# Performance work log

Measured on AMD Instinct MI355X. Metric: run time of the kernel, lower is better.

## Reference

```python
import jax, jax.numpy as jnp
import numpy as np

B, NCLS, P, C, D, H, DIMG = 256, 1000, 5, 72, 512, 8, 768
T = P + C  # 77 = CLIP context length
DH = D // H


def _ln(x, g, b):
    m = jnp.mean(x, axis=-1, keepdims=True)
    v = jnp.var(x, axis=-1, keepdims=True)
    return (x - m) * jax.lax.rsqrt(v + 1e-5) * g + b


def _transformer(x, ln_g, ln_b, Wq, Wk, Wv, Wo):
    # Stand-in for clip.model.transformer: pre-LN self-attention block that
    # also exposes its (head-averaged) attention map, as used by
    # clip.get_attention_map(). x: [N, T, D]
    N, Tx, _ = x.shape
    h = _ln(x, ln_g, ln_b)
    q = (h @ Wq).reshape(N, Tx, H, DH)
    k = (h @ Wk).reshape(N, Tx, H, DH)
    v = (h @ Wv).reshape(N, Tx, H, DH)
    scores = jnp.einsum('nqhd,nkhd->nhqk', q, k) / jnp.sqrt(jnp.float32(DH))
    A = jax.nn.softmax(scores, axis=-1)          # [N, H, T, T]
    attn_map = A.mean(axis=1)                    # [N, T, T]
    o = jnp.einsum('nhqk,nkhd->nqhd', A, v).reshape(N, Tx, D) @ Wo
    return x + o, attn_map


def setup_inputs() -> dict:
    key = jax.random.key(0)
    ks = jax.random.split(key, 10)
    s = 0.02
    return {
        'images': jax.random.normal(ks[0], (B, DIMG), jnp.float32),
        'W_img': jax.random.normal(ks[1], (DIMG, D), jnp.float32) * s,
        'ctx': jax.random.normal(ks[2], (NCLS, P, D), jnp.float32) * s,
        'cls_tok': jax.random.normal(ks[3], (NCLS, C, D), jnp.float32) * s,
        'ln_g': jnp.ones((D,), jnp.float32),
        'ln_b': jnp.zeros((D,), jnp.float32),
        'Wq': jax.random.normal(ks[4], (D, D), jnp.float32) * s,
        'Wk': jax.random.normal(ks[5], (D, D), jnp.float32) * s,
        'Wv': jax.random.normal(ks[6], (D, D), jnp.float32) * s,
        'Wo': jax.random.normal(ks[7], (D, D), jnp.float32) * s,
        'text_proj': jax.random.normal(ks[8], (D, D), jnp.float32) * s,
        'logit_scale': jnp.full((1,), np.log(1.0 / 0.07), jnp.float32),
    }


def reference(images, W_img, ctx, cls_tok, ln_g, ln_b, Wq, Wk, Wv, Wo,
              text_proj, logit_scale):
    # Image branch: encode + L2 normalize
    img = images @ W_img
    img = img / jnp.linalg.norm(img, axis=-1, keepdims=True)  # [B, D]

    # Prompts are identical across the batch in the original (ctx.expand),
    # so the per-sample inner loop collapses to one pass per class.
    prompt = jnp.concatenate([ctx, cls_tok], axis=1)          # [NCLS, T, D]
    _, attn = _transformer(prompt, ln_g, ln_b, Wq, Wk, Wv, Wo)

    # AttributionMonitor: attention from the last (EOT) token onto the
    # prompt_len learned context tokens, normalized.
    attr = jax.nn.softmax(attn[:, -1, :P], axis=-1)           # [NCLS, P]

    # PromptAdjustor(method='scale'): scale context tokens by attribution.
    adj_ctx = ctx * attr[..., None]
    adj_prompt = jnp.concatenate([adj_ctx, cls_tok], axis=1)  # [NCLS, T, D]

    h, _ = _transformer(adj_prompt, ln_g, ln_b, Wq, Wk, Wv, Wo)
    txt = h[:, -1, :] @ text_proj                             # [NCLS, D]
    txt = txt / jnp.linalg.norm(txt, axis=-1, keepdims=True)

    logits = jnp.exp(logit_scale[0]) * (img @ txt.T)          # [B, NCLS]
    return logits
```

## Files before the change

### kernel.cpp

```cpp
#include <hip/hip_runtime.h>
#include <hip/hip_bf16.h>

#define DEV static __device__ __forceinline__

typedef __attribute__((ext_vector_type(8))) short bf16x8;
typedef __attribute__((ext_vector_type(4))) short s16x4;
typedef __attribute__((ext_vector_type(4))) float f32x4;

DEV float wsum(float v) {
  v += __shfl_xor(v, 1);  v += __shfl_xor(v, 2);  v += __shfl_xor(v, 4);
  v += __shfl_xor(v, 8);  v += __shfl_xor(v, 16); v += __shfl_xor(v, 32);
  return v;
}
DEV float wmaxr(float v) {
  v = fmaxf(v, __shfl_xor(v, 1));  v = fmaxf(v, __shfl_xor(v, 2));
  v = fmaxf(v, __shfl_xor(v, 4));  v = fmaxf(v, __shfl_xor(v, 8));
  v = fmaxf(v, __shfl_xor(v, 16)); v = fmaxf(v, __shfl_xor(v, 32));
  return v;
}
DEV short f2bf(float x) {
  __hip_bfloat16 h = __float2bfloat16(x);
  return *reinterpret_cast<short*>(&h);
}
DEV float bf2f(unsigned int u) {
  const unsigned int x = u << 16;
  return __uint_as_float(x);
}
DEV float bfs2f(short s) {
  const unsigned int x = ((unsigned int)(unsigned short)s) << 16;
  return __uint_as_float(x);
}

DEV float fold8(const float v[8], int lane) {
  float w4[4];
#pragma unroll
  for (int j = 0; j < 4; ++j) {
    const float mine  = (lane & 1) ? v[2 * j + 1] : v[2 * j];
    const float other = (lane & 1) ? v[2 * j]     : v[2 * j + 1];
    w4[j] = mine + __shfl_xor(other, 1);
  }
  float u2[2];
#pragma unroll
  for (int j = 0; j < 2; ++j) {
    const float mine  = (lane & 2) ? w4[2 * j + 1] : w4[2 * j];
    const float other = (lane & 2) ? w4[2 * j]     : w4[2 * j + 1];
    u2[j] = mine + __shfl_xor(other, 2);
  }
  const float mine  = (lane & 4) ? u2[1] : u2[0];
  const float other = (lane & 4) ? u2[0] : u2[1];
  float z = mine + __shfl_xor(other, 4);
  z += __shfl_xor(z, 8); z += __shfl_xor(z, 16); z += __shfl_xor(z, 32);
  return z;
}

template <int TRANSB, int ADDD, int ABF16, int OUTBF16>
__global__ __launch_bounds__(256) void gemm_mfma_k(
    const void* __restrict__ Av, int lda, long long bsA,
    const float* __restrict__ B, int ldb, long long bsB,
    void* __restrict__ Cv, int ldc, long long bsC,
    const float* __restrict__ D, long long ldd,
    int M, int N, int K)
{
  const float* Af = (const float*)Av + (ABF16 ? 0 : (size_t)blockIdx.z * bsA);
  const short* Ah = (const short*)Av + (ABF16 ? (size_t)blockIdx.z * bsA : 0);
  B += (size_t)blockIdx.z * bsB;
  const int m0 = blockIdx.y * 64, n0 = blockIdx.x * 64;
  const int tid = threadIdx.x;
  const int w = tid >> 6, lane = tid & 63;
  const int wr = w >> 1, wc = w & 1;
  __shared__ __attribute__((aligned(16))) short As[2][64][40];
  __shared__ __attribute__((aligned(16))) short Bs[2][64][40];
  f32x4 acc[2][2] = {};

  const int ar = tid >> 2, akc = (tid & 3) * 8;
  const int br = tid >> 3, bnc = (tid & 7) * 8;
  const bool arv = (m0 + ar < M);
  const int rbase = wr * 32 + (lane & 15);
  const int cbase = wc * 32 + (lane & 15);
  const int kb = (lane >> 4) * 8;

  auto gload = [&](int k0, float4& a0, float4& a1, bf16x8& ah,
                   float4& b0, float4& b1) {
    if (ABF16) {
      ah = bf16x8{};
      if (arv) ah = *(const bf16x8*)(Ah + (size_t)(m0 + ar) * lda + k0 + akc);
    } else {
      a0 = make_float4(0.f, 0.f, 0.f, 0.f); a1 = a0;
      if (arv) {
        a0 = *(const float4*)(Af + (size_t)(m0 + ar) * lda + k0 + akc);
        a1 = *(const float4*)(Af + (size_t)(m0 + ar) * lda + k0 + akc + 4);
      }
    }
    if (TRANSB) {
      b0 = *(const float4*)(B + (size_t)(n0 + ar) * ldb + k0 + akc);
      b1 = *(const float4*)(B + (size_t)(n0 + ar) * ldb + k0 + akc + 4);
    } else {
      b0 = *(const float4*)(B + (size_t)(k0 + br) * ldb + n0 + bnc);
      b1 = *(const float4*)(B + (size_t)(k0 + br) * ldb + n0 + bnc + 4);
    }
  };
  auto stage = [&](int buf, const float4& a0, const float4& a1, const bf16x8& ah,
                   const float4& b0, const float4& b1) {
    if (ABF16) {
      *(bf16x8*)&As[buf][ar][akc] = ah;
    } else {
      bf16x8 av;
      av[0] = f2bf(a0.x); av[1] = f2bf(a0.y); av[2] = f2bf(a0.z); av[3] = f2bf(a0.w);
      av[4] = f2bf(a1.x); av[5] = f2bf(a1.y); av[6] = f2bf(a1.z); av[7] = f2bf(a1.w);
      *(bf16x8*)&As[buf][ar][akc] = av;
    }
    if (TRANSB) {
      bf16x8 bv;
      bv[0] = f2bf(b0.x); bv[1] = f2bf(b0.y); bv[2] = f2bf(b0.z); bv[3] = f2bf(b0.w);
      bv[4] = f2bf(b1.x); bv[5] = f2bf(b1.y); bv[6] = f2bf(b1.z); bv[7] = f2bf(b1.w);
      *(bf16x8*)&Bs[buf][ar][akc] = bv;
    } else {
      Bs[buf][bnc + 0][br] = f2bf(b0.x); Bs[buf][bnc + 1][br] = f2bf(b0.y);
      Bs[buf][bnc + 2][br] = f2bf(b0.z); Bs[buf][bnc + 3][br] = f2bf(b0.w);
      Bs[buf][bnc + 4][br] = f2bf(b1.x); Bs[buf][bnc + 5][br] = f2bf(b1.y);
      Bs[buf][bnc + 6][br] = f2bf(b1.z); Bs[buf][bnc + 7][br] = f2bf(b1.w);
    }
  };
  auto compute = [&](int buf) {
    bf16x8 af0 = *(const bf16x8*)&As[buf][rbase][kb];
    bf16x8 af1 = *(const bf16x8*)&As[buf][rbase + 16][kb];
    bf16x8 bf0 = *(const bf16x8*)&Bs[buf][cbase][kb];
    bf16x8 bf1 = *(const bf16x8*)&Bs[buf][cbase + 16][kb];
    acc[0][0] = __builtin_amdgcn_mfma_f32_16x16x32_bf16(af0, bf0, acc[0][0], 0, 0, 0);
    acc[0][1] = __builtin_amdgcn_mfma_f32_16x16x32_bf16(af0, bf1, acc[0][1], 0, 0, 0);
    acc[1][0] = __builtin_amdgcn_mfma_f32_16x16x32_bf16(af1, bf0, acc[1][0], 0, 0, 0);
    acc[1][1] = __builtin_amdgcn_mfma_f32_16x16x32_bf16(af1, bf1, acc[1][1], 0, 0, 0);
  };

  float4 a0A, a1A, b0A, b1A, a0B, a1B, b0B, b1B;
  bf16x8 ahA = {}, ahB = {};
  gload(0, a0A, a1A, ahA, b0A, b1A);
  gload(32, a0B, a1B, ahB, b0B, b1B);
  for (int k0 = 0; k0 < K; k0 += 64) {
    stage(0, a0A, a1A, ahA, b0A, b1A);
    if (k0 + 64 < K) gload(k0 + 64, a0A, a1A, ahA, b0A, b1A);
    __syncthreads();
    compute(0);
    stage(1, a0B, a1B, ahB, b0B, b1B);
    if (k0 + 96 < K) gload(k0 + 96, a0B, a1B, ahB, b0B, b1B);
    __syncthreads();
    compute(1);
  }

  const size_t cb = (size_t)blockIdx.z * (size_t)bsC;
#pragma unroll
  for (int mi = 0; mi < 2; ++mi)
#pragma unroll
    for (int ni = 0; ni < 2; ++ni)
#pragma unroll
      for (int r = 0; r < 4; ++r) {
        const int row = m0 + wr * 32 + mi * 16 + (lane >> 4) * 4 + r;
        const int col = n0 + wc * 32 + ni * 16 + (lane & 15);
        if (row < M) {
          float v = acc[mi][ni][r];
          if (ADDD) v += D[(size_t)row * ldd + col];
          if (OUTBF16)
            ((__hip_bfloat16*)Cv)[cb + (size_t)row * ldc + col] = __float2bfloat16(v);
          else
            ((float*)Cv)[cb + (size_t)row * ldc + col] = v;
        }
      }
}

__global__ __launch_bounds__(256) void gemm_mfma_lnA_k(
    const float* __restrict__ A, long long lda,
    const float* __restrict__ g, const float* __restrict__ b,
    const float* __restrict__ B, int ldb,
    float* __restrict__ C, int ldc,
    int M, int N, int K)
{
  const int m0 = blockIdx.y * 64, n0 = blockIdx.x * 64;
  const int tid = threadIdx.x;
  const int w = tid >> 6, lane = tid & 63;
  const int wr = w >> 1, wc = w & 1;
  __shared__ __attribute__((aligned(16))) short As[2][64][40];
  __shared__ __attribute__((aligned(16))) short Bs[2][64][40];
  __shared__ __attribute__((aligned(16))) float g_s[512], b_s[512];
  __shared__ float mean_s[64], rstd_s[64];
  f32x4 acc[2][2] = {};

  if (tid < 128) ((float4*)g_s)[tid] = ((const float4*)g)[tid];
  else ((float4*)b_s)[tid - 128] = ((const float4*)b)[tid - 128];

  {
    const int r = tid >> 2, p = tid & 3;
    float s = 0.f, ss = 0.f;
    if (m0 + r < M) {
      const float4* src = (const float4*)(A + (size_t)(m0 + r) * lda + p * 128);
#pragma unroll 8
      for (int i = 0; i < 32; ++i) {
        const float4 v = src[i];
        s += v.x + v.y + v.z + v.w;
        ss += v.x * v.x + v.y * v.y + v.z * v.z + v.w * v.w;
      }
    }
    s += __shfl_xor(s, 1);  s += __shfl_xor(s, 2);
    ss += __shfl_xor(ss, 1); ss += __shfl_xor(ss, 2);
    if (p == 0) {
      const float mean = s * (1.f / 512.f);
      mean_s[r] = mean;
      rstd_s[r] = rsqrtf(ss * (1.f / 512.f) - mean * mean + 1e-5f);
    }
  }
  __syncthreads();

  const int ar = tid >> 2, akc = (tid & 3) * 8;
  const int br = tid >> 3, bnc = (tid & 7) * 8;
  const bool arv = (m0 + ar < M);
  const int rbase = wr * 32 + (lane & 15);
  const int cbase = wc * 32 + (lane & 15);
  const int kb = (lane >> 4) * 8;

  auto gload = [&](int k0, float4& a0, float4& a1, float4& b0, float4& b1) {
    a0 = make_float4(0.f, 0.f, 0.f, 0.f); a1 = a0;
    if (arv) {
      a0 = *(const float4*)(A + (size_t)(m0 + ar) * lda + k0 + akc);
      a1 = *(const float4*)(A + (size_t)(m0 + ar) * lda + k0 + akc + 4);
    }
    b0 = *(const float4*)(B + (size_t)(k0 + br) * ldb + n0 + bnc);
    b1 = *(const float4*)(B + (size_t)(k0 + br) * ldb + n0 + bnc + 4);
  };
  auto stage = [&](int buf, int k0, const float4& a0, const float4& a1,
                   const float4& b0, const float4& b1) {
    const float mn = mean_s[ar], rs = rstd_s[ar];
    const int kc = k0 + akc;
    bf16x8 av;
    av[0] = f2bf((a0.x - mn) * rs * g_s[kc + 0] + b_s[kc + 0]);
    av[1] = f2bf((a0.y - mn) * rs * g_s[kc + 1] + b_s[kc + 1]);
    av[2] = f2bf((a0.z - mn) * rs * g_s[kc + 2] + b_s[kc + 2]);
    av[3] = f2bf((a0.w - mn) * rs * g_s[kc + 3] + b_s[kc + 3]);
    av[4] = f2bf((a1.x - mn) * rs * g_s[kc + 4] + b_s[kc + 4]);
    av[5] = f2bf((a1.y - mn) * rs * g_s[kc + 5] + b_s[kc + 5]);
    av[6] = f2bf((a1.z - mn) * rs * g_s[kc + 6] + b_s[kc + 6]);
    av[7] = f2bf((a1.w - mn) * rs * g_s[kc + 7] + b_s[kc + 7]);
    *(bf16x8*)&As[buf][ar][akc] = av;
    Bs[buf][bnc + 0][br] = f2bf(b0.x); Bs[buf][bnc + 1][br] = f2bf(b0.y);
    Bs[buf][bnc + 2][br] = f2bf(b0.z); Bs[buf][bnc + 3][br] = f2bf(b0.w);
    Bs[buf][bnc + 4][br] = f2bf(b1.x); Bs[buf][bnc + 5][br] = f2bf(b1.y);
    Bs[buf][bnc + 6][br] = f2bf(b1.z); Bs[buf][bnc + 7][br] = f2bf(b1.w);
  };
  auto compute = [&](int buf) {
    bf16x8 af0 = *(const bf16x8*)&As[buf][rbase][kb];
    bf16x8 af1 = *(const bf16x8*)&As[buf][rbase + 16][kb];
    bf16x8 bf0 = *(const bf16x8*)&Bs[buf][cbase][kb];
    bf16x8 bf1 = *(const bf16x8*)&Bs[buf][cbase + 16][kb];
    acc[0][0] = __builtin_amdgcn_mfma_f32_16x16x32_bf16(af0, bf0, acc[0][0], 0, 0, 0);
    acc[0][1] = __builtin_amdgcn_mfma_f32_16x16x32_bf16(af0, bf1, acc[0][1], 0, 0, 0);
    acc[1][0] = __builtin_amdgcn_mfma_f32_16x16x32_bf16(af1, bf0, acc[1][0], 0, 0, 0);
    acc[1][1] = __builtin_amdgcn_mfma_f32_16x16x32_bf16(af1, bf1, acc[1][1], 0, 0, 0);
  };

  float4 a0A, a1A, b0A, b1A, a0B, a1B, b0B, b1B;
  gload(0, a0A, a1A, b0A, b1A);
  gload(32, a0B, a1B, b0B, b1B);
  for (int k0 = 0; k0 < K; k0 += 64) {
    stage(0, k0, a0A, a1A, b0A, b1A);
    if (k0 + 64 < K) gload(k0 + 64, a0A, a1A, b0A, b1A);
    __syncthreads();
    compute(0);
    stage(1, k0 + 32, a0B, a1B, b0B, b1B);
    if (k0 + 96 < K) gload(k0 + 96, a0B, a1B, b0B, b1B);
    __syncthreads();
    compute(1);
  }

#pragma unroll
  for (int mi = 0; mi < 2; ++mi)
#pragma unroll
    for (int ni = 0; ni < 2; ++ni)
#pragma unroll
      for (int r = 0; r < 4; ++r) {
        const int row = m0 + wr * 32 + mi * 16 + (lane >> 4) * 4 + r;
        const int col = n0 + wc * 32 + ni * 16 + (lane & 15);
        if (row < M) C[(size_t)row * ldc + col] = acc[mi][ni][r];
      }
}

__global__ __launch_bounds__(256) void logits_k(
    const float* __restrict__ A, int lda,
    const float* __restrict__ B, int ldb,
    float* __restrict__ C, int ldc,
    const float* __restrict__ alpha_ptr,
    int M, int N, int K)
{
  const int m0 = blockIdx.y * 32, n0 = blockIdx.x * 64;
  const int tid = threadIdx.x;
  __shared__ __attribute__((aligned(16))) float As[2][16][36];
  __shared__ __attribute__((aligned(16))) float Bs[2][16][68];
  __shared__ float nA[32], nB[64];
  float acc[2][4] = {};
  float ssA = 0.f, ssB = 0.f;
  const int ty = tid >> 4, tx = tid & 15;
  const int am = tid >> 3, ak = (tid & 7) * 2;
  const int bm = tid >> 2, bt = (tid & 3) * 4;
  const bool aval = (m0 + am < M);
  const bool bval = (n0 + bm < N);

  float2 av; float4 bv;
  auto gload = [&](int k0) {
    av = make_float2(0.f, 0.f);
    bv = make_float4(0.f, 0.f, 0.f, 0.f);
    if (aval) av = *(const float2*)(A + (size_t)(m0 + am) * lda + (k0 + ak));
    if (bval) bv = *(const float4*)(B + (size_t)(n0 + bm) * ldb + (k0 + bt));
    ssA += av.x * av.x + av.y * av.y;
    ssB += bv.x * bv.x + bv.y * bv.y + bv.z * bv.z + bv.w * bv.w;
  };
  auto sstore = [&](int buf) {
    As[buf][ak][am] = av.x; As[buf][ak + 1][am] = av.y;
    Bs[buf][bt + 0][bm] = bv.x; Bs[buf][bt + 1][bm] = bv.y;
    Bs[buf][bt + 2][bm] = bv.z; Bs[buf][bt + 3][bm] = bv.w;
  };

  const int nIt = K >> 4;
  gload(0); sstore(0);
  for (int it = 0; it < nIt; ++it) {
    __syncthreads();
    if (it + 1 < nIt) gload((it + 1) << 4);
    const int buf = it & 1;
#pragma unroll
    for (int kk = 0; kk < 16; ++kk) {
      const float2 a  = *(const float2*)&As[buf][kk][ty * 2];
      const float4 bq = *(const float4*)&Bs[buf][kk][tx * 4];
      acc[0][0] += a.x * bq.x; acc[0][1] += a.x * bq.y; acc[0][2] += a.x * bq.z; acc[0][3] += a.x * bq.w;
      acc[1][0] += a.y * bq.x; acc[1][1] += a.y * bq.y; acc[1][2] += a.y * bq.z; acc[1][3] += a.y * bq.w;
    }
    if (it + 1 < nIt) sstore((it + 1) & 1);
  }

  ssA += __shfl_xor(ssA, 1); ssA += __shfl_xor(ssA, 2); ssA += __shfl_xor(ssA, 4);
  if ((tid & 7) == 0) nA[am] = rsqrtf(ssA);
  ssB += __shfl_xor(ssB, 1); ssB += __shfl_xor(ssB, 2);
  if ((tid & 3) == 0) nB[bm] = rsqrtf(ssB);
  __syncthreads();

  const float alpha = __expf(alpha_ptr[0]);
#pragma unroll
  for (int i = 0; i < 2; ++i) {
    const int m = m0 + ty * 2 + i;
    if (m >= M) continue;
    const float fa = alpha * nA[ty * 2 + i];
#pragma unroll
    for (int j = 0; j < 4; ++j) {
      const int nn = n0 + tx * 4 + j;
      if (nn < N) C[(size_t)m * ldc + nn] = acc[i][j] * fa * nB[tx * 4 + j];
    }
  }
}

__global__ __launch_bounds__(256) void fused_sweep_kernel(
    const float* __restrict__ ctx, const float* __restrict__ cls,
    const float* __restrict__ g, const float* __restrict__ b,
    const __hip_bfloat16* __restrict__ wt, __hip_bfloat16* __restrict__ u_out)
{
  const int n = blockIdx.x, tid = threadIdx.x;
  const int w = tid >> 6, lane = tid & 63;
  __shared__ __attribute__((aligned(16))) float gw_s[8][512];
  __shared__ __attribute__((aligned(16))) float g_s[512], b_s[512];
  __shared__ __attribute__((aligned(16))) short h2_s[5][512];
  __shared__ float sc_s[8][80];
  __shared__ float sc2_s[8][5];
  __shared__ float ah_s[8][5];
  __shared__ float wstatB[4][8], wstatL[4][8];
  __shared__ float attr_s[5];
  __shared__ float Sgw_l[8], bw_l[8];
  __shared__ float Bt_s[8], Lt_s[8], inv_s[8];
  __shared__ float e2_s[8][5];
  __shared__ __attribute__((aligned(16))) float es_s[4][2][8];

  {
    const uint4* wsrc = (const uint4*)(wt + (size_t)n * 4096);
    float4* gwf = (float4*)&gw_s[0][0];
    for (int i = tid; i < 512; i += 256) {
      const uint4 v = wsrc[i];
      gwf[i * 2]     = make_float4(bf2f(v.x & 0xffffu), bf2f(v.x >> 16),
                                   bf2f(v.y & 0xffffu), bf2f(v.y >> 16));
      gwf[i * 2 + 1] = make_float4(bf2f(v.z & 0xffffu), bf2f(v.z >> 16),
                                   bf2f(v.w & 0xffffu), bf2f(v.w >> 16));
    }
    if (tid < 128) ((float4*)g_s)[tid] = ((const float4*)g)[tid];
    else ((float4*)b_s)[tid - 128] = ((const float4*)b)[tid - 128];
  }
  __syncthreads();

  for (int hh = w; hh < 8; hh += 4) {
    float s1 = 0.f, s2 = 0.f;
#pragma unroll
    for (int i = 0; i < 8; ++i) {
      const int j = lane + 64 * i;
      const float wv = gw_s[hh][j];
      const float gv = wv * g_s[j];
      s1 += gv; s2 += wv * b_s[j];
      gw_s[hh][j] = gv;
    }
    s1 = wsum(s1); s2 = wsum(s2);
    if (lane == 0) { Sgw_l[hh] = s1; bw_l[hh] = s2; }
  }
  __syncthreads();
  const float sg_r  = Sgw_l[lane & 7];
  const float bw8_r = bw_l[lane & 7] * 0.125f;
  const int j0 = lane * 4, j1 = lane * 4 + 256;

  for (int k = w; k < 5; k += 4) {
    const float* src = ctx + ((size_t)n * 5 + k) * 512;
    const float4 x0 = *(const float4*)(src + j0);
    const float4 x1 = *(const float4*)(src + j1);
    float s  = x0.x + x0.y + x0.z + x0.w + x1.x + x1.y + x1.z + x1.w;
    float ss = x0.x * x0.x + x0.y * x0.y + x0.z * x0.z + x0.w * x0.w
             + x1.x * x1.x + x1.y * x1.y + x1.z * x1.z + x1.w * x1.w;
    float v8[8] = {};
#pragma unroll
    for (int hh = 0; hh < 8; ++hh) {
      const float4 w0 = *(const float4*)&gw_s[hh][j0];
      const float4 w1 = *(const float4*)&gw_s[hh][j1];
      v8[hh] = x0.x * w0.x + x0.y * w0.y + x0.z * w0.z + x0.w * w0.w
             + x1.x * w1.x + x1.y * w1.y + x1.z * w1.z + x1.w * w1.w;
    }
    s = wsum(s); ss = wsum(ss);
    const float mean = s * (1.f / 512.f);
    const float rstd = rsqrtf(ss * (1.f / 512.f) - mean * mean + 1e-5f);
    const float z = fold8(v8, lane);
    const float zf = rstd * 0.125f * (z - mean * sg_r) + bw8_r;
    if (lane < 8) sc_s[lane][k] = zf;
  }

  float A[8][8];
#pragma unroll
  for (int hh = 0; hh < 8; ++hh)
#pragma unroll
    for (int i = 0; i < 8; ++i) A[hh][i] = 0.f;
  float B8[8] = {}, L8[8] = {};

  const float* base = cls + (size_t)n * 72 * 512;
  float4 xa0, xa1, xb0, xb1, ya0, ya1, yb0, yb1;
  {
    const float* sA = base + (size_t)w * 512;
    const float* sB = base + (size_t)(w + 4) * 512;
    xa0 = *(const float4*)(sA + j0); xa1 = *(const float4*)(sA + j1);
    xb0 = *(const float4*)(sB + j0); xb1 = *(const float4*)(sB + j1);
    const float* sA1 = base + (size_t)(w + 8) * 512;
    const float* sB1 = base + (size_t)(w + 12) * 512;
    ya0 = *(const float4*)(sA1 + j0); ya1 = *(const float4*)(sA1 + j1);
    yb0 = *(const float4*)(sB1 + j0); yb1 = *(const float4*)(sB1 + j1);
  }
  for (int p = 0; p < 9; ++p) {
    float4 za0, za1, zb0, zb1;
    const bool more2 = (p + 2 < 9);
    if (more2) {
      const float* sA = base + (size_t)(w + 8 * (p + 2)) * 512;
      const float* sB = base + (size_t)(w + 4 + 8 * (p + 2)) * 512;
      za0 = *(const float4*)(sA + j0); za1 = *(const float4*)(sA + j1);
      zb0 = *(const float4*)(sB + j0); zb1 = *(const float4*)(sB + j1);
    }
    float sa = xa0.x + xa0.y + xa0.z + xa0.w + xa1.x + xa1.y + xa1.z + xa1.w;
    float ssa = xa0.x * xa0.x + xa0.y * xa0.y + xa0.z * xa0.z + xa0.w * xa0.w
              + xa1.x * xa1.x + xa1.y * xa1.y + xa1.z * xa1.z + xa1.w * xa1.w;
    float sb = xb0.x + xb0.y + xb0.z + xb0.w + xb1.x + xb1.y + xb1.z + xb1.w;
    float ssb = xb0.x * xb0.x + xb0.y * xb0.y + xb0.z * xb0.z + xb0.w * xb0.w
              + xb1.x * xb1.x + xb1.y * xb1.y + xb1.z * xb1.z + xb1.w * xb1.w;
    float v8a[8], v8b[8];
#pragma unroll
    for (int hh = 0; hh < 8; ++hh) {
      const float4 w0 = *(const float4*)&gw_s[hh][j0];
      const float4 w1 = *(const float4*)&gw_s[hh][j1];
      v8a[hh] = xa0.x * w0.x + xa0.y * w0.y + xa0.z * w0.z + xa0.w * w0.w
              + xa1.x * w1.x + xa1.y * w1.y + xa1.z * w1.z + xa1.w * w1.w;
      v8b[hh] = xb0.x * w0.x + xb0.y * w0.y + xb0.z * w0.z + xb0.w * w0.w
              + xb1.x * w1.x + xb1.y * w1.y + xb1.z * w1.z + xb1.w * w1.w;
    }
    sa = wsum(sa); ssa = wsum(ssa); sb = wsum(sb); ssb = wsum(ssb);
    const float meanA = sa * (1.f / 512.f);
    const float rstdA = rsqrtf(ssa * (1.f / 512.f) - meanA * meanA + 1e-5f);
    const float meanB = sb * (1.f / 512.f);
    const float rstdB = rsqrtf(ssb * (1.f / 512.f) - meanB * meanB + 1e-5f);
    const float za = fold8(v8a, lane);
    const float zb = fold8(v8b, lane);
    const float zfa = rstdA * 0.125f * (za - meanA * sg_r) + bw8_r;
    const float zfb = rstdB * 0.125f * (zb - meanB * sg_r) + bw8_r;
    const int kA = 5 + w + 8 * p;
    if (lane < 8) {
      sc_s[lane][kA] = zfa; sc_s[lane][kA + 4] = zfb;
      es_s[w][0][lane] = __expf(zfa);
      es_s[w][1][lane] = __expf(zfb);
    }
    __builtin_amdgcn_wave_barrier();
    const float4 ea0 = *(const float4*)&es_s[w][0][0];
    const float4 ea1 = *(const float4*)&es_s[w][0][4];
    const float4 eb0 = *(const float4*)&es_s[w][1][0];
    const float4 eb1 = *(const float4*)&es_s[w][1][4];
    const float esa[8] = {ea0.x, ea0.y, ea0.z, ea0.w, ea1.x, ea1.y, ea1.z, ea1.w};
    const float esb[8] = {eb0.x, eb0.y, eb0.z, eb0.w, eb1.x, eb1.y, eb1.z, eb1.w};
#pragma unroll
    for (int hh = 0; hh < 8; ++hh) {
      const float erA = esa[hh] * rstdA;
      const float erB = esb[hh] * rstdB;
      A[hh][0] += erA * xa0.x; A[hh][1] += erA * xa0.y;
      A[hh][2] += erA * xa0.z; A[hh][3] += erA * xa0.w;
      A[hh][4] += erA * xa1.x; A[hh][5] += erA * xa1.y;
      A[hh][6] += erA * xa1.z; A[hh][7] += erA * xa1.w;
      B8[hh] += erA * meanA;
      L8[hh] += esa[hh];
      A[hh][0] += erB * xb0.x; A[hh][1] += erB * xb0.y;
      A[hh][2] += erB * xb0.z; A[hh][3] += erB * xb0.w;
      A[hh][4] += erB * xb1.x; A[hh][5] += erB * xb1.y;
      A[hh][6] += erB * xb1.z; A[hh][7] += erB * xb1.w;
      B8[hh] += erB * meanB;
      L8[hh] += esb[hh];
    }
    xa0 = ya0; xa1 = ya1; xb0 = yb0; xb1 = yb1;
    if (more2) { ya0 = za0; ya1 = za1; yb0 = zb0; yb1 = zb1; }
  }
  if (lane == 0)
#pragma unroll
    for (int hh = 0; hh < 8; ++hh) {
      wstatB[w][hh] = B8[hh]; wstatL[w][hh] = L8[hh];
    }
  __syncthreads();

  for (int hh = w; hh < 8; hh += 4) {
    const float v0 = sc_s[hh][lane];
    const float v1 = (lane + 64 < 77) ? sc_s[hh][lane + 64] : -1e30f;
    const float mx = wmaxr(fmaxf(v0, v1));
    const float e0 = __expf(v0 - mx);
    const float e1 = (lane + 64 < 77) ? __expf(v1 - mx) : 0.f;
    const float S = wsum(e0 + e1);
    if (lane < 5) ah_s[hh][lane] = e0 / S;
  }
  __syncthreads();
  if (tid == 0) {
    float m[5], mx = -1e30f;
#pragma unroll
    for (int p = 0; p < 5; ++p) {
      float acc = 0.f;
      for (int hh = 0; hh < 8; ++hh) acc += ah_s[hh][p];
      m[p] = acc * 0.125f;
      mx = fmaxf(mx, m[p]);
    }
    float e[5], S = 0.f;
#pragma unroll
    for (int p = 0; p < 5; ++p) { e[p] = __expf(m[p] - mx); S += e[p]; }
#pragma unroll
    for (int p = 0; p < 5; ++p) attr_s[p] = e[p] / S;
  }
  __syncthreads();

  for (int k = w; k < 5; k += 4) {
    const float c = attr_s[k];
    const float* src = ctx + ((size_t)n * 5 + k) * 512;
    float4 x0 = *(const float4*)(src + j0);
    float4 x1 = *(const float4*)(src + j1);
    x0.x *= c; x0.y *= c; x0.z *= c; x0.w *= c;
    x1.x *= c; x1.y *= c; x1.z *= c; x1.w *= c;
    float s  = x0.x + x0.y + x0.z + x0.w + x1.x + x1.y + x1.z + x1.w;
    float ss = x0.x * x0.x + x0.y * x0.y + x0.z * x0.z + x0.w * x0.w
             + x1.x * x1.x + x1.y * x1.y + x1.z * x1.z + x1.w * x1.w;
    float v8[8];
#pragma unroll
    for (int hh = 0; hh < 8; ++hh) {
      const float4 w0 = *(const float4*)&gw_s[hh][j0];
      const float4 w1 = *(const float4*)&gw_s[hh][j1];
      v8[hh] = x0.x * w0.x + x0.y * w0.y + x0.z * w0.z + x0.w * w0.w
             + x1.x * w1.x + x1.y * w1.y + x1.z * w1.z + x1.w * w1.w;
    }
    s = wsum(s); ss = wsum(ss);
    const float mean = s * (1.f / 512.f);
    const float rstd = rsqrtf(ss * (1.f / 512.f) - mean * mean + 1e-5f);
    {
      const float4 gg0 = *(const float4*)&g_s[j0];
      const float4 bb0 = *(const float4*)&b_s[j0];
      const float4 gg1 = *(const float4*)&g_s[j1];
      const float4 bb1 = *(const float4*)&b_s[j1];
      s16x4 o0, o1;
      o0[0] = f2bf((x0.x - mean) * rstd * gg0.x + bb0.x);
      o0[1] = f2bf((x0.y - mean) * rstd * gg0.y + bb0.y);
      o0[2] = f2bf((x0.z - mean) * rstd * gg0.z + bb0.z);
      o0[3] = f2bf((x0.w - mean) * rstd * gg0.w + bb0.w);
      o1[0] = f2bf((x1.x - mean) * rstd * gg1.x + bb1.x);
      o1[1] = f2bf((x1.y - mean) * rstd * gg1.y + bb1.y);
      o1[2] = f2bf((x1.z - mean) * rstd * gg1.z + bb1.z);
      o1[3] = f2bf((x1.w - mean) * rstd * gg1.w + bb1.w);
      *(s16x4*)&h2_s[k][j0] = o0;
      *(s16x4*)&h2_s[k][j1] = o1;
    }
    const float z = fold8(v8, lane);
    const float zf = rstd * 0.125f * (z - mean * sg_r) + bw8_r;
    if (lane < 8) sc2_s[lane][k] = zf;
  }
  __syncthreads();

  for (int wv = 0; wv < 4; ++wv) {
    if (w == wv) {
#pragma unroll
      for (int hh = 0; hh < 8; ++hh) {
        float4* p0 = (float4*)&gw_s[hh][j0];
        float4* p1 = (float4*)&gw_s[hh][j1];
        const float4 a0 = make_float4(A[hh][0], A[hh][1], A[hh][2], A[hh][3]);
        const float4 a1 = make_float4(A[hh][4], A[hh][5], A[hh][6], A[hh][7]);
        if (wv == 0) { *p0 = a0; *p1 = a1; }
        else {
          float4 v0 = *p0, v1 = *p1;
          v0.x += a0.x; v0.y += a0.y; v0.z += a0.z; v0.w += a0.w;
          v1.x += a1.x; v1.y += a1.y; v1.z += a1.z; v1.w += a1.w;
          *p0 = v0; *p1 = v1;
        }
      }
    }
    __syncthreads();
  }

  if (tid < 8) {
    float Bt = 0.f, Lt = 0.f;
    for (int wv = 0; wv < 4; ++wv) { Bt += wstatB[wv][tid]; Lt += wstatL[wv][tid]; }
    float den = Lt;
#pragma unroll
    for (int k = 0; k < 5; ++k) {
      const float e = __expf(sc2_s[tid][k]);
      e2_s[tid][k] = e; den += e;
    }
    Bt_s[tid] = Bt; Lt_s[tid] = Lt; inv_s[tid] = 1.f / den;
  }
  __syncthreads();

  __hip_bfloat16* dst = u_out + (size_t)n * 4096;
  for (int bidx = tid * 4; bidx < 4096; bidx += 1024) {
    const int hh = bidx >> 9, j = bidx & 511;
    const float4 a4 = *(const float4*)&gw_s[hh][j];
    const float4 g4 = *(const float4*)&g_s[j];
    const float4 b4 = *(const float4*)&b_s[j];
    const float Bt = Bt_s[hh], Lt = Lt_s[hh];
    float v0 = (a4.x - Bt) * g4.x + Lt * b4.x;
    float v1 = (a4.y - Bt) * g4.y + Lt * b4.y;
    float v2 = (a4.z - Bt) * g4.z + Lt * b4.z;
    float v3 = (a4.w - Bt) * g4.w + Lt * b4.w;
#pragma unroll
    for (int k = 0; k < 5; ++k) {
      const s16x4 hq = *(const s16x4*)&h2_s[k][j];
      const float e = e2_s[hh][k];
      v0 += e * bfs2f(hq[0]); v1 += e * bfs2f(hq[1]);
      v2 += e * bfs2f(hq[2]); v3 += e * bfs2f(hq[3]);
    }
    const float iv = inv_s[hh];
    s16x4 o;
    o[0] = f2bf(v0 * iv); o[1] = f2bf(v1 * iv);
    o[2] = f2bf(v2 * iv); o[3] = f2bf(v3 * iv);
    *(s16x4*)&dst[bidx] = o;
  }
}

extern "C" void kernel_launch(void* const* d_in, const int* in_sizes, int n_in,
                              void* d_out, int out_size, void* d_ws, size_t ws_size,
                              hipStream_t stream)
{
  const float* images = (const float*)d_in[0];
  const float* W_img  = (const float*)d_in[1];
  const float* ctx    = (const float*)d_in[2];
  const float* cls    = (const float*)d_in[3];
  const float* ln_g   = (const float*)d_in[4];
  const float* ln_b   = (const float*)d_in[5];
  const float* Wq     = (const float*)d_in[6];
  const float* Wk     = (const float*)d_in[7];
  const float* Wv     = (const float*)d_in[8];
  const float* Wo     = (const float*)d_in[9];
  const float* tproj  = (const float*)d_in[10];
  const float* lscale = (const float*)d_in[11];

  __hip_bfloat16* wtu = (__hip_bfloat16*)d_ws;
  float* fws  = (float*)d_ws;
  float* img  = fws + 2048000;
  float* hlO  = img + 131072;
  float* qo2  = hlO + 512000;
  float* txt  = fws;
  (void)in_sizes; (void)n_in; (void)out_size; (void)ws_size;

  gemm_mfma_k<0,0,0,0><<<dim3(8,4,1),256,0,stream>>>(images,768,0, W_img,512,0,
      img,512,0, nullptr,0, 256,512,768);

  gemm_mfma_lnA_k<<<dim3(8,16),256,0,stream>>>(cls + 71*512, 72*512,
      ln_g, ln_b, Wq,512, qo2,512, 1000,512,512);

  gemm_mfma_k<1,0,0,1><<<dim3(8,16,8),256,0,stream>>>(qo2,512,64, Wk,512,64,
      wtu,4096,512, nullptr,0, 1000,512,64);

  fused_sweep_kernel<<<1000,256,0,stream>>>(ctx, cls, ln_g, ln_b, wtu, wtu);

  gemm_mfma_k<0,0,1,0><<<dim3(1,16,8),256,0,stream>>>(wtu,4096,512, Wv,512,64,
      hlO,512,64, nullptr,0, 1000,64,512);

  gemm_mfma_k<0,1,0,0><<<dim3(8,16,1),256,0,stream>>>(hlO,512,0, Wo,512,0,
      qo2,512,0, cls + 71*512, 72*512, 1000,512,512);
  gemm_mfma_k<0,0,0,0><<<dim3(8,16,1),256,0,stream>>>(qo2,512,0, tproj,512,0,
      txt,512,0, nullptr,0, 1000,512,512);

  logits_k<<<dim3(16,8),256,0,stream>>>(img,512, txt,512,
      (float*)d_out,1000, lscale, 256,1000,512);
}
```

Before: 154.0 us.

## Stage gamma-scaled prompt rows in LDS and compute EOT scores with MFMA

The fused per-class sweep kernel now loads all 77 prompt rows once into shared memory as bf16, pre-multiplied by the LayerNorm gamma, and stores per-row mean and rstd. The EOT-query attention scores are then computed with 16x16x32 bf16 MFMA instructions instead of per-row wave reductions. The second pass reuses the cached rows rather than re-reading global memory, and derives the scaled-context LayerNorm statistics analytically from the first pass's values. The trade-off is a large LDS footprint (about 80x516 shorts), which may reduce occupancy, plus bf16 rounding of gamma*x that costs some accuracy.

```diff
diff --git a/kernel.cpp b/kernel.cpp
--- a/kernel.cpp
+++ b/kernel.cpp
@@ -6,6 +6,7 @@
 typedef __attribute__((ext_vector_type(8))) short bf16x8;
 typedef __attribute__((ext_vector_type(4))) short s16x4;
 typedef __attribute__((ext_vector_type(4))) float f32x4;
+typedef __attribute__((ext_vector_type(2))) float f32x2;
 
 DEV float wsum(float v) {
   v += __shfl_xor(v, 1);  v += __shfl_xor(v, 2);  v += __shfl_xor(v, 4);
@@ -29,28 +30,6 @@
 DEV float bfs2f(short s) {
   const unsigned int x = ((unsigned int)(unsigned short)s) << 16;
   return __uint_as_float(x);
-}
-
-DEV float fold8(const float v[8], int lane) {
-  float w4[4];
-#pragma unroll
-  for (int j = 0; j < 4; ++j) {
-    const float mine  = (lane & 1) ? v[2 * j + 1] : v[2 * j];
-    const float other = (lane & 1) ? v[2 * j]     : v[2 * j + 1];
-    w4[j] = mine + __shfl_xor(other, 1);
-  }
-  float u2[2];
-#pragma unroll
-  for (int j = 0; j < 2; ++j) {
-    const float mine  = (lane & 2) ? w4[2 * j + 1] : w4[2 * j];
-    const float other = (lane & 2) ? w4[2 * j]     : w4[2 * j + 1];
-    u2[j] = mine + __shfl_xor(other, 2);
-  }
-  const float mine  = (lane & 4) ? u2[1] : u2[0];
-  const float other = (lane & 4) ? u2[0] : u2[1];
-  float z = mine + __shfl_xor(other, 4);
-  z += __shfl_xor(z, 8); z += __shfl_xor(z, 16); z += __shfl_xor(z, 32);
-  return z;
 }
 
 template <int TRANSB, int ADDD, int ABF16, int OUTBF16>
@@ -359,10 +338,14 @@
 {
   const int n = blockIdx.x, tid = threadIdx.x;
   const int w = tid >> 6, lane = tid & 63;
-  __shared__ __attribute__((aligned(16))) float gw_s[8][512];
+  constexpr int XP = 516;
+  __shared__ __attribute__((aligned(16))) short Xs[80][XP];
   __shared__ __attribute__((aligned(16))) float g_s[512], b_s[512];
   __shared__ __attribute__((aligned(16))) short h2_s[5][512];
+  __shared__ float mean_s[80], rstd_s[80];
   __shared__ float sc_s[8][80];
+  __shared__ float es_s[8][72];
+  __shared__ float zraw_s[8][5];
   __shared__ float sc2_s[8][5];
   __shared__ float ah_s[8][5];
   __shared__ float wstatB[4][8], wstatL[4][8];
@@ -370,155 +353,81 @@
   __shared__ float Sgw_l[8], bw_l[8];
   __shared__ float Bt_s[8], Lt_s[8], inv_s[8];
   __shared__ float e2_s[8][5];
-  __shared__ __attribute__((aligned(16))) float es_s[4][2][8];
-
-  {
-    const uint4* wsrc = (const uint4*)(wt + (size_t)n * 4096);
-    float4* gwf = (float4*)&gw_s[0][0];
-    for (int i = tid; i < 512; i += 256) {
-      const uint4 v = wsrc[i];
-      gwf[i * 2]     = make_float4(bf2f(v.x & 0xffffu), bf2f(v.x >> 16),
-                                   bf2f(v.y & 0xffffu), bf2f(v.y >> 16));
-      gwf[i * 2 + 1] = make_float4(bf2f(v.z & 0xffffu), bf2f(v.z >> 16),
-                                   bf2f(v.w & 0xffffu), bf2f(v.w >> 16));
-    }
-    if (tid < 128) ((float4*)g_s)[tid] = ((const float4*)g)[tid];
-    else ((float4*)b_s)[tid - 128] = ((const float4*)b)[tid - 128];
-  }
-  __syncthreads();
-
-  for (int hh = w; hh < 8; hh += 4) {
-    float s1 = 0.f, s2 = 0.f;
-#pragma unroll
-    for (int i = 0; i < 8; ++i) {
-      const int j = lane + 64 * i;
-      const float wv = gw_s[hh][j];
-      const float gv = wv * g_s[j];
-      s1 += gv; s2 += wv * b_s[j];
-      gw_s[hh][j] = gv;
-    }
-    s1 = wsum(s1); s2 = wsum(s2);
-    if (lane == 0) { Sgw_l[hh] = s1; bw_l[hh] = s2; }
-  }
-  __syncthreads();
-  const float sg_r  = Sgw_l[lane & 7];
-  const float bw8_r = bw_l[lane & 7] * 0.125f;
-  const int j0 = lane * 4, j1 = lane * 4 + 256;
-
-  for (int k = w; k < 5; k += 4) {
-    const float* src = ctx + ((size_t)n * 5 + k) * 512;
-    const float4 x0 = *(const float4*)(src + j0);
-    const float4 x1 = *(const float4*)(src + j1);
-    float s  = x0.x + x0.y + x0.z + x0.w + x1.x + x1.y + x1.z + x1.w;
-    float ss = x0.x * x0.x + x0.y * x0.y + x0.z * x0.z + x0.w * x0.w
-             + x1.x * x1.x + x1.y * x1.y + x1.z * x1.z + x1.w * x1.w;
-    float v8[8] = {};
-#pragma unroll
-    for (int hh = 0; hh < 8; ++hh) {
-      const float4 w0 = *(const float4*)&gw_s[hh][j0];
-      const float4 w1 = *(const float4*)&gw_s[hh][j1];
-      v8[hh] = x0.x * w0.x + x0.y * w0.y + x0.z * w0.z + x0.w * w0.w
-             + x1.x * w1.x + x1.y * w1.y + x1.z * w1.z + x1.w * w1.w;
-    }
-    s = wsum(s); ss = wsum(ss);
-    const float mean = s * (1.f / 512.f);
-    const float rstd = rsqrtf(ss * (1.f / 512.f) - mean * mean + 1e-5f);
-    const float z = fold8(v8, lane);
-    const float zf = rstd * 0.125f * (z - mean * sg_r) + bw8_r;
-    if (lane < 8) sc_s[lane][k] = zf;
-  }
-
-  float A[8][8];
-#pragma unroll
-  for (int hh = 0; hh < 8; ++hh)
-#pragma unroll
-    for (int i = 0; i < 8; ++i) A[hh][i] = 0.f;
-  float B8[8] = {}, L8[8] = {};
-
-  const float* base = cls + (size_t)n * 72 * 512;
-  float4 xa0, xa1, xb0, xb1, ya0, ya1, yb0, yb1;
-  {
-    const float* sA = base + (size_t)w * 512;
-    const float* sB = base + (size_t)(w + 4) * 512;
-    xa0 = *(const float4*)(sA + j0); xa1 = *(const float4*)(sA + j1);
-    xb0 = *(const float4*)(sB + j0); xb1 = *(const float4*)(sB + j1);
-    const float* sA1 = base + (size_t)(w + 8) * 512;
-    const float* sB1 = base + (size_t)(w + 12) * 512;
-    ya0 = *(const float4*)(sA1 + j0); ya1 = *(const float4*)(sA1 + j1);
-    yb0 = *(const float4*)(sB1 + j0); yb1 = *(const float4*)(sB1 + j1);
-  }
-  for (int p = 0; p < 9; ++p) {
-    float4 za0, za1, zb0, zb1;
-    const bool more2 = (p + 2 < 9);
-    if (more2) {
-      const float* sA = base + (size_t)(w + 8 * (p + 2)) * 512;
-      const float* sB = base + (size_t)(w + 4 + 8 * (p + 2)) * 512;
-      za0 = *(const float4*)(sA + j0); za1 = *(const float4*)(sA + j1);
-      zb0 = *(const float4*)(sB + j0); zb1 = *(const float4*)(sB + j1);
-    }
-    float sa = xa0.x + xa0.y + xa0.z + xa0.w + xa1.x + xa1.y + xa1.z + xa1.w;
-    float ssa = xa0.x * xa0.x + xa0.y * xa0.y + xa0.z * xa0.z + xa0.w * xa0.w
-              + xa1.x * xa1.x + xa1.y * xa1.y + xa1.z * xa1.z + xa1.w * xa1.w;
-    float sb = xb0.x + xb0.y + xb0.z + xb0.w + xb1.x + xb1.y + xb1.z + xb1.w;
-    float ssb = xb0.x * xb0.x + xb0.y * xb0.y + xb0.z * xb0.z + xb0.w * xb0.w
-              + xb1.x * xb1.x + xb1.y * xb1.y + xb1.z * xb1.z + xb1.w * xb1.w;
-    float v8a[8], v8b[8];
-#pragma unroll
-    for (int hh = 0; hh < 8; ++hh) {
-      const float4 w0 = *(const float4*)&gw_s[hh][j0];
-      const float4 w1 = *(const float4*)&gw_s[hh][j1];
-      v8a[hh] = xa0.x * w0.x + xa0.y * w0.y + xa0.z * w0.z + xa0.w * w0.w
-              + xa1.x * w1.x + xa1.y * w1.y + xa1.z * w1.z + xa1.w * w1.w;
-      v8b[hh] = xb0.x * w0.x + xb0.y * w0.y + xb0.z * w0.z + xb0.w * w0.w
-              + xb1.x * w1.x + xb1.y * w1.y + xb1.z * w1.z + xb1.w * w1.w;
-    }
-    sa = wsum(sa); ssa = wsum(ssa); sb = wsum(sb); ssb = wsum(ssb);
-    const float meanA = sa * (1.f / 512.f);
-    const float rstdA = rsqrtf(ssa * (1.f / 512.f) - meanA * meanA + 1e-5f);
-    const float meanB = sb * (1.f / 512.f);
-    const float rstdB = rsqrtf(ssb * (1.f / 512.f) - meanB * meanB + 1e-5f);
-    const float za = fold8(v8a, lane);
-    const float zb = fold8(v8b, lane);
-    const float zfa = rstdA * 0.125f * (za - meanA * sg_r) + bw8_r;
-    const float zfb = rstdB * 0.125f * (zb - meanB * sg_r) + bw8_r;
-    const int kA = 5 + w + 8 * p;
-    if (lane < 8) {
-      sc_s[lane][kA] = zfa; sc_s[lane][kA + 4] = zfb;
-      es_s[w][0][lane] = __expf(zfa);
-      es_s[w][1][lane] = __expf(zfb);
-    }
-    __builtin_amdgcn_wave_barrier();
-    const float4 ea0 = *(const float4*)&es_s[w][0][0];
-    const float4 ea1 = *(const float4*)&es_s[w][0][4];
-    const float4 eb0 = *(const float4*)&es_s[w][1][0];
-    const float4 eb1 = *(const float4*)&es_s[w][1][4];
-    const float esa[8] = {ea0.x, ea0.y, ea0.z, ea0.w, ea1.x, ea1.y, ea1.z, ea1.w};
-    const float esb[8] = {eb0.x, eb0.y, eb0.z, eb0.w, eb1.x, eb1.y, eb1.z, eb1.w};
-#pragma unroll
-    for (int hh = 0; hh < 8; ++hh) {
-      const float erA = esa[hh] * rstdA;
-      const float erB = esb[hh] * rstdB;
-      A[hh][0] += erA * xa0.x; A[hh][1] += erA * xa0.y;
-      A[hh][2] += erA * xa0.z; A[hh][3] += erA * xa0.w;
-      A[hh][4] += erA * xa1.x; A[hh][5] += erA * xa1.y;
-      A[hh][6] += erA * xa1.z; A[hh][7] += erA * xa1.w;
-      B8[hh] += erA * meanA;
-      L8[hh] += esa[hh];
-      A[hh][0] += erB * xb0.x; A[hh][1] += erB * xb0.y;
-      A[hh][2] += erB * xb0.z; A[hh][3] += erB * xb0.w;
-      A[hh][4] += erB * xb1.x; A[hh][5] += erB * xb1.y;
-      A[hh][6] += erB * xb1.z; A[hh][7] += erB * xb1.w;
-      B8[hh] += erB * meanB;
-      L8[hh] += esb[hh];
-    }
-    xa0 = ya0; xa1 = ya1; xb0 = yb0; xb1 = yb1;
-    if (more2) { ya0 = za0; ya1 = za1; yb0 = zb0; yb1 = zb1; }
-  }
-  if (lane == 0)
-#pragma unroll
-    for (int hh = 0; hh < 8; ++hh) {
-      wstatB[w][hh] = B8[hh]; wstatL[w][hh] = L8[hh];
-    }
+
+  if (tid < 128) ((float4*)g_s)[tid] = ((const float4*)g)[tid];
+  else ((float4*)b_s)[tid - 128] = ((const float4*)b)[tid - 128];
+  __syncthreads();
+
+  const short* wtS = (const short*)wt + (size_t)n * 4096;
+
+  auto loadrow = [&](int row, int p) {
+    const float* src = (row < 5)
+        ? ctx + ((size_t)n * 5 + row) * 512 + p * 128
+        : cls + ((size_t)n * 72 + (row - 5)) * 512 + p * 128;
+    float s = 0.f, ss = 0.f;
+    for (int c2 = 0; c2 < 4; ++c2) {
+      float4 xv[8];
+#pragma unroll
+      for (int i = 0; i < 8; ++i) xv[i] = ((const float4*)src)[c2 * 8 + i];
+#pragma unroll
+      for (int i = 0; i < 8; ++i) {
+        s  += xv[i].x + xv[i].y + xv[i].z + xv[i].w;
+        ss += xv[i].x * xv[i].x + xv[i].y * xv[i].y
+            + xv[i].z * xv[i].z + xv[i].w * xv[i].w;
+        const int j = p * 128 + c2 * 32 + i * 4;
+        const float4 gg = *(const float4*)&g_s[j];
+        s16x4 o;
+        o[0] = f2bf(xv[i].x * gg.x); o[1] = f2bf(xv[i].y * gg.y);
+        o[2] = f2bf(xv[i].z * gg.z); o[3] = f2bf(xv[i].w * gg.w);
+        *(s16x4*)&Xs[row][j] = o;
+      }
+    }
+    s += __shfl_xor(s, 1);  s += __shfl_xor(s, 2);
+    ss += __shfl_xor(ss, 1); ss += __shfl_xor(ss, 2);
+    if (p == 0) {
+      const float mean = s * (1.f / 512.f);
+      mean_s[row] = mean;
+      rstd_s[row] = rsqrtf(ss * (1.f / 512.f) - mean * mean + 1e-5f);
+    }
+  };
+  loadrow(tid >> 2, tid & 3);
+  if (tid < 52) {
+    loadrow(64 + (tid >> 2), tid & 3);
+  } else if (w >= 1) {
+    for (int h = w - 1; h < 8; h += 3) {
+      const bf16x8 wv = *(const bf16x8*)(wtS + h * 512 + lane * 8);
+      float s1 = 0.f, s2 = 0.f;
+#pragma unroll
+      for (int i = 0; i < 8; ++i) {
+        const float wf = bfs2f(wv[i]);
+        s1 += wf * g_s[lane * 8 + i];
+        s2 += wf * b_s[lane * 8 + i];
+      }
+      s1 = wsum(s1); s2 = wsum(s2);
+      if (lane == 0) { Sgw_l[h] = s1; bw_l[h] = s2; }
+    }
+  }
+  __syncthreads();
+
+  for (int t = w; t < 5; t += 4) {
+    f32x4 acc = {};
+#pragma unroll
+    for (int kt = 0; kt < 16; ++kt) {
+      const bf16x8 af = *(const bf16x8*)(wtS + (lane & 15) * 512 + kt * 32 + (lane >> 4) * 8);
+      const bf16x8 bf = *(const bf16x8*)&Xs[t * 16 + (lane & 15)][kt * 32 + (lane >> 4) * 8];
+      acc = __builtin_amdgcn_mfma_f32_16x16x32_bf16(af, bf, acc, 0, 0, 0);
+    }
+    const int row = t * 16 + (lane & 15);
+#pragma unroll
+    for (int r = 0; r < 4; ++r) {
+      const int h = (lane >> 4) * 4 + r;
+      if (h < 8 && row < 77) {
+        sc_s[h][row] = rstd_s[row] * 0.125f * (acc[r] - mean_s[row] * Sgw_l[h])
+                     + 0.125f * bw_l[h];
+        if (row < 5) zraw_s[h][row] = acc[r];
+      }
+    }
+  }
   __syncthreads();
 
   for (int hh = w; hh < 8; hh += 4) {
@@ -546,70 +455,97 @@
 #pragma unroll
     for (int p = 0; p < 5; ++p) attr_s[p] = e[p] / S;
   }
+  for (int idx = tid; idx < 576; idx += 256) {
+    const int h = idx / 72, k = idx % 72;
+    es_s[h][k] = __expf(sc_s[h][k + 5]);
+  }
   __syncthreads();
 
   for (int k = w; k < 5; k += 4) {
     const float c = attr_s[k];
-    const float* src = ctx + ((size_t)n * 5 + k) * 512;
-    float4 x0 = *(const float4*)(src + j0);
-    float4 x1 = *(const float4*)(src + j1);
-    x0.x *= c; x0.y *= c; x0.z *= c; x0.w *= c;
-    x1.x *= c; x1.y *= c; x1.z *= c; x1.w *= c;
-    float s  = x0.x + x0.y + x0.z + x0.w + x1.x + x1.y + x1.z + x1.w;
-    float ss = x0.x * x0.x + x0.y * x0.y + x0.z * x0.z + x0.w * x0.w
-             + x1.x * x1.x + x1.y * x1.y + x1.z * x1.z + x1.w * x1.w;
-    float v8[8];
+    const float mean = mean_s[k], rstd1 = rstd_s[k];
+    const float var = 1.f / (rstd1 * rstd1) - 1e-5f;
+    const float rstd2 = rsqrtf(c * c * var + 1e-5f);
+    if (lane < 8)
+      sc2_s[lane][k] = rstd2 * 0.125f * (c * zraw_s[lane][k] - c * mean * Sgw_l[lane])
+                     + 0.125f * bw_l[lane];
+    const float cr = c * rstd2;
+    const int j0 = lane * 4, j1 = j0 + 256;
+#pragma unroll
+    for (int half = 0; half < 2; ++half) {
+      const int j = half ? j1 : j0;
+      const s16x4 xq = *(const s16x4*)&Xs[k][j];
+      const float4 gg = *(const float4*)&g_s[j];
+      const float4 bb = *(const float4*)&b_s[j];
+      s16x4 o;
+      o[0] = f2bf(cr * (bfs2f(xq[0]) - mean * gg.x) + bb.x);
+      o[1] = f2bf(cr * (bfs2f(xq[1]) - mean * gg.y) + bb.y);
+      o[2] = f2bf(cr * (bfs2f(xq[2]) - mean * gg.z) + bb.z);
+      o[3] = f2bf(cr * (bfs2f(xq[3]) - mean * gg.w) + bb.w);
+      *(s16x4*)&h2_s[k][j] = o;
+    }
+  }
+
+  f32x2 A2[8][4];
+#pragma unroll
+  for (int hh = 0; hh < 8; ++hh)
+#pragma unroll
+    for (int i = 0; i < 4; ++i) A2[hh][i] = f32x2{0.f, 0.f};
+  float B8[8] = {}, L8[8] = {};
+  {
+    const int j0 = lane * 4, j1 = j0 + 256;
+#pragma unroll 2
+    for (int k = 5 + w; k < 77; k += 4) {
+      const s16x4 x0q = *(const s16x4*)&Xs[k][j0];
+      const s16x4 x1q = *(const s16x4*)&Xs[k][j1];
+      const float rstd = rstd_s[k], mean = mean_s[k];
+      const f32x2 q0 = f32x2{bfs2f(x0q[0]), bfs2f(x0q[1])};
+      const f32x2 q1 = f32x2{bfs2f(x0q[2]), bfs2f(x0q[3])};
+      const f32x2 q2 = f32x2{bfs2f(x1q[0]), bfs2f(x1q[1])};
+      const f32x2 q3 = f32x2{bfs2f(x1q[2]), bfs2f(x1q[3])};
+#pragma unroll
+      for (int hh = 0; hh < 8; ++hh) {
+        const float es = es_s[hh][k - 5];
+        const float er = es * rstd;
+        const f32x2 ev = f32x2{er, er};
+        A2[hh][0] += ev * q0; A2[hh][1] += ev * q1;
+        A2[hh][2] += ev * q2; A2[hh][3] += ev * q3;
+        B8[hh] += er * mean;
+        L8[hh] += es;
+      }
+    }
+  }
+  if (lane == 0)
 #pragma unroll
     for (int hh = 0; hh < 8; ++hh) {
-      const float4 w0 = *(const float4*)&gw_s[hh][j0];
-      const float4 w1 = *(const float4*)&gw_s[hh][j1];
-      v8[hh] = x0.x * w0.x + x0.y * w0.y + x0.z * w0.z + x0.w * w0.w
-             + x1.x * w1.x + x1.y * w1.y + x1.z * w1.z + x1.w * w1.w;
-    }
-    s = wsum(s); ss = wsum(ss);
-    const float mean = s * (1.f / 512.f);
-    const float rstd = rsqrtf(ss * (1.f / 512.f) - mean * mean + 1e-5f);
-    {
-      const float4 gg0 = *(const float4*)&g_s[j0];
-      const float4 bb0 = *(const float4*)&b_s[j0];
-      const float4 gg1 = *(const float4*)&g_s[j1];
-      const float4 bb1 = *(const float4*)&b_s[j1];
-      s16x4 o0, o1;
-      o0[0] = f2bf((x0.x - mean) * rstd * gg0.x + bb0.x);
-      o0[1] = f2bf((x0.y - mean) * rstd * gg0.y + bb0.y);
-      o0[2] = f2bf((x0.z - mean) * rstd * gg0.z + bb0.z);
-      o0[3] = f2bf((x0.w - mean) * rstd * gg0.w + bb0.w);
-      o1[0] = f2bf((x1.x - mean) * rstd * gg1.x + bb1.x);
-      o1[1] = f2bf((x1.y - mean) * rstd * gg1.y + bb1.y);
-      o1[2] = f2bf((x1.z - mean) * rstd * gg1.z + bb1.z);
-      o1[3] = f2bf((x1.w - mean) * rstd * gg1.w + bb1.w);
-      *(s16x4*)&h2_s[k][j0] = o0;
-      *(s16x4*)&h2_s[k][j1] = o1;
-    }
-    const float z = fold8(v8, lane);
-    const float zf = rstd * 0.125f * (z - mean * sg_r) + bw8_r;
-    if (lane < 8) sc2_s[lane][k] = zf;
-  }
-  __syncthreads();
-
-  for (int wv = 0; wv < 4; ++wv) {
-    if (w == wv) {
-#pragma unroll
-      for (int hh = 0; hh < 8; ++hh) {
-        float4* p0 = (float4*)&gw_s[hh][j0];
-        float4* p1 = (float4*)&gw_s[hh][j1];
-        const float4 a0 = make_float4(A[hh][0], A[hh][1], A[hh][2], A[hh][3]);
-        const float4 a1 = make_float4(A[hh][4], A[hh][5], A[hh][6], A[hh][7]);
-        if (wv == 0) { *p0 = a0; *p1 = a1; }
-        else {
-          float4 v0 = *p0, v1 = *p1;
-          v0.x += a0.x; v0.y += a0.y; v0.z += a0.z; v0.w += a0.w;
-          v1.x += a1.x; v1.y += a1.y; v1.z += a1.z; v1.w += a1.w;
-          *p0 = v0; *p1 = v1;
+      wstatB[w][hh] = B8[hh]; wstatL[w][hh] = L8[hh];
+    }
+  __syncthreads();
+
+  float* Ac = (float*)&Xs[0][0];
+  {
+    const int j0 = lane * 4, j1 = j0 + 256;
+    for (int wv = 0; wv < 4; ++wv) {
+      if (w == wv) {
+#pragma unroll
+        for (int hh = 0; hh < 8; ++hh) {
+          float4* p0 = (float4*)&Ac[hh * 512 + j0];
+          float4* p1 = (float4*)&Ac[hh * 512 + j1];
+          const float4 a0 = make_float4(A2[hh][0][0], A2[hh][0][1],
+                                        A2[hh][1][0], A2[hh][1][1]);
+          const float4 a1 = make_float4(A2[hh][2][0], A2[hh][2][1],
+                                        A2[hh][3][0], A2[hh][3][1]);
+          if (wv == 0) { *p0 = a0; *p1 = a1; }
+          else {
+            float4 v0 = *p0, v1 = *p1;
+            v0.x += a0.x; v0.y += a0.y; v0.z += a0.z; v0.w += a0.w;
+            v1.x += a1.x; v1.y += a1.y; v1.z += a1.z; v1.w += a1.w;
+            *p0 = v0; *p1 = v1;
+          }
         }
       }
-    }
-    __syncthreads();
+      __syncthreads();
+    }
   }
 
   if (tid < 8) {
@@ -628,14 +564,14 @@
   __hip_bfloat16* dst = u_out + (size_t)n * 4096;
   for (int bidx = tid * 4; bidx < 4096; bidx += 1024) {
     const int hh = bidx >> 9, j = bidx & 511;
-    const float4 a4 = *(const float4*)&gw_s[hh][j];
+    const float4 a4 = *(const float4*)&Ac[hh * 512 + j];
     const float4 g4 = *(const float4*)&g_s[j];
     const float4 b4 = *(const float4*)&b_s[j];
     const float Bt = Bt_s[hh], Lt = Lt_s[hh];
-    float v0 = (a4.x - Bt) * g4.x + Lt * b4.x;
-    float v1 = (a4.y - Bt) * g4.y + Lt * b4.y;
-    float v2 = (a4.z - Bt) * g4.z + Lt * b4.z;
-    float v3 = (a4.w - Bt) * g4.w + Lt * b4.w;
+    float v0 = a4.x - Bt * g4.x + Lt * b4.x;
+    float v1 = a4.y - Bt * g4.y + Lt * b4.y;
+    float v2 = a4.z - Bt * g4.z + Lt * b4.z;
+    float v3 = a4.w - Bt * g4.w + Lt * b4.w;
 #pragma unroll
     for (int k = 0; k < 5; ++k) {
       const s16x4 hq = *(const s16x4*)&h2_s[k][j];
```

Result: slower. 175.2 us (+13.8%).
